# Kernel optimization log

Hardware: AMD Instinct MI355X
Metric: run time of the kernel (lower is better)

The kernel has to match this reference:

```python
import jax, jax.numpy as jnp
import numpy as np

N_NODES = 50000
NEG_SLOPE = 0.2
EPS = 1e-16


def _gat_layer(x, src, dst, W, a_src, a_dst, b, concat):
    """One PyG-style GATConv layer (eval mode, self-loops already in src/dst).
    x: [N, F_in], W: [F_in, H*C], a_src/a_dst: [H, C], b: [H*C] or [C].
    """
    H, C = a_src.shape
    N = x.shape[0]
    h = (x @ W).reshape(N, H, C)                      # [N, H, C]
    alpha_s = jnp.einsum('nhc,hc->nh', h, a_src)      # [N, H]
    alpha_d = jnp.einsum('nhc,hc->nh', h, a_dst)      # [N, H]
    e = alpha_s[src] + alpha_d[dst]                   # [E, H]
    e = jax.nn.leaky_relu(e, NEG_SLOPE)
    # segment softmax over edges grouped by destination node
    m = jax.ops.segment_max(e, dst, num_segments=N)   # [N, H]
    e = jnp.exp(e - m[dst])
    denom = jax.ops.segment_sum(e, dst, num_segments=N)
    alpha = e / (denom[dst] + EPS)                    # [E, H]
    msg = h[src] * alpha[:, :, None]                  # [E, H, C]
    out = jax.ops.segment_sum(msg, dst, num_segments=N)  # [N, H, C]
    if concat:
        out = out.reshape(N, H * C)
    else:
        out = out.mean(axis=1)
    return out + b


def setup_inputs() -> dict:
    key = jax.random.key(0)
    ks = jax.random.split(key, 16)
    N, E = N_NODES, 800000
    in_dim, hid, heads = 128, 64, 2
    x = jax.random.normal(ks[0], (N, in_dim), dtype=jnp.float32)
    edge_index = jax.random.randint(ks[1], (2, E), 0, N, dtype=jnp.int64)
    s = 0.1
    return {
        'x': x,
        'edge_index': edge_index,
        # layer 0: in_dim -> hid, heads
        'W0': s * jax.random.normal(ks[2], (in_dim, heads * hid), dtype=jnp.float32),
        'as0': s * jax.random.normal(ks[3], (heads, hid), dtype=jnp.float32),
        'ad0': s * jax.random.normal(ks[4], (heads, hid), dtype=jnp.float32),
        'b0': jnp.zeros((heads * hid,), dtype=jnp.float32),
        # layer 1: hid*heads -> hid, heads
        'W1': s * jax.random.normal(ks[5], (heads * hid, heads * hid), dtype=jnp.float32),
        'as1': s * jax.random.normal(ks[6], (heads, hid), dtype=jnp.float32),
        'ad1': s * jax.random.normal(ks[7], (heads, hid), dtype=jnp.float32),
        'b1': jnp.zeros((heads * hid,), dtype=jnp.float32),
        # layer 2: hid*heads -> hid, heads=1
        'W2': s * jax.random.normal(ks[8], (heads * hid, hid), dtype=jnp.float32),
        'as2': s * jax.random.normal(ks[9], (1, hid), dtype=jnp.float32),
        'ad2': s * jax.random.normal(ks[10], (1, hid), dtype=jnp.float32),
        'b2': jnp.zeros((hid,), dtype=jnp.float32),
    }


def reference(x, edge_index, W0, as0, ad0, b0, W1, as1, ad1, b1, W2, as2, ad2, b2):
    N = x.shape[0]
    # PyG GATConv default add_self_loops=True
    loop = jnp.arange(N, dtype=edge_index.dtype)
    src = jnp.concatenate([edge_index[0], loop])
    dst = jnp.concatenate([edge_index[1], loop])
    h = _gat_layer(x, src, dst, W0, as0, ad0, b0, concat=True)
    h = jax.nn.relu(h)
    h = _gat_layer(h, src, dst, W1, as1, ad1, b1, concat=True)
    h = jax.nn.relu(h)
    out = _gat_layer(h, src, dst, W2, as2, ad2, b2, concat=True)  # heads=1: concat == identity
    return out
```

## Files before the change

kernel.cpp:

```cpp
#include <hip/hip_runtime.h>
#include <hip/hip_fp16.h>

#define NEG_SLOPE 0.2f
#define EPSF 1e-16f

typedef _Float16 half8 __attribute__((ext_vector_type(8)));
typedef float floatx4 __attribute__((ext_vector_type(4)));

__global__ void to_half_kernel(const float* __restrict__ in, __half* __restrict__ out,
                               int n8) {
    int i = blockIdx.x * blockDim.x + threadIdx.x;
    if (i < n8) {
        float4 a = ((const float4*)in)[i * 2];
        float4 b = ((const float4*)in)[i * 2 + 1];
        __half2 hp[4];
        hp[0] = __floats2half2_rn(a.x, a.y);
        hp[1] = __floats2half2_rn(a.z, a.w);
        hp[2] = __floats2half2_rn(b.x, b.y);
        hp[3] = __floats2half2_rn(b.z, b.w);
        ((uint4*)out)[i] = *(uint4*)hp;
    }
}

template<int BN, int HEADS>
__global__ __launch_bounds__(256) void gemm_mfma(const __half* __restrict__ X,
                                                 const float* __restrict__ W,
                                                 const float* __restrict__ asrc,
                                                 const float* __restrict__ adst,
                                                 __half* __restrict__ OutH,
                                                 float* __restrict__ AS,
                                                 float* __restrict__ AD, int N) {
    constexpr int KP = 136;
    constexpr int NF = BN / 16;
    __shared__ _Float16 Wt[BN][KP];
    const int tid = threadIdx.x;
    const int wave = tid >> 6, lane = tid & 63;
    const int r = lane & 15;
    const int g = lane >> 4;
    const int row0 = blockIdx.x * 64 + wave * 16;

    for (int idx = tid; idx < 128 * (BN / 4); idx += 256) {
        int k = idx / (BN / 4), n4 = idx % (BN / 4);
        float4 w4 = *(const float4*)&W[(size_t)k * BN + n4 * 4];
        Wt[n4 * 4 + 0][k] = (_Float16)w4.x;
        Wt[n4 * 4 + 1][k] = (_Float16)w4.y;
        Wt[n4 * 4 + 2][k] = (_Float16)w4.z;
        Wt[n4 * 4 + 3][k] = (_Float16)w4.w;
    }
    __syncthreads();

    const int arow = row0 + r;
    const int arow_c = (arow < N) ? arow : (N - 1);

    floatx4 acc[NF];
#pragma unroll
    for (int n = 0; n < NF; ++n) acc[n] = (floatx4)(0.f);

#pragma unroll
    for (int ks = 0; ks < 4; ++ks) {
        half8 afrag = *(const half8*)&X[(size_t)arow_c * 128 + ks * 32 + g * 8];
#pragma unroll
        for (int n = 0; n < NF; ++n) {
            half8 bfrag = *(const half8*)&Wt[n * 16 + r][ks * 32 + g * 8];
            acc[n] = __builtin_amdgcn_mfma_f32_16x16x32_f16(afrag, bfrag, acc[n], 0, 0, 0);
        }
    }

    float av[NF], dv[NF];
#pragma unroll
    for (int n = 0; n < NF; ++n) { av[n] = asrc[n * 16 + r]; dv[n] = adst[n * 16 + r]; }

#pragma unroll
    for (int reg = 0; reg < 4; ++reg) {
        const int orow = row0 + g * 4 + reg;
        if (orow >= N) continue;
#pragma unroll
        for (int n = 0; n < NF; ++n)
            OutH[(size_t)orow * BN + n * 16 + r] = __float2half(acc[n][reg]);
        float ps0 = 0.f, pd0 = 0.f, ps1 = 0.f, pd1 = 0.f;
#pragma unroll
        for (int n = 0; n < NF; ++n) {
            float v = acc[n][reg];
            if (HEADS == 2 && n >= NF / 2) { ps1 = fmaf(v, av[n], ps1); pd1 = fmaf(v, dv[n], pd1); }
            else                           { ps0 = fmaf(v, av[n], ps0); pd0 = fmaf(v, dv[n], pd0); }
        }
#pragma unroll
        for (int o = 1; o < 16; o <<= 1) {
            ps0 += __shfl_xor(ps0, o, 64); pd0 += __shfl_xor(pd0, o, 64);
            if (HEADS == 2) { ps1 += __shfl_xor(ps1, o, 64); pd1 += __shfl_xor(pd1, o, 64); }
        }
        if (r == 0) {
            if (HEADS == 2) {
                AS[orow * 2] = ps0; AS[orow * 2 + 1] = ps1;
                AD[orow * 2] = pd0; AD[orow * 2 + 1] = pd1;
            } else {
                AS[orow] = ps0; AD[orow] = pd0;
            }
        }
    }
}

__global__ void zero_kernel(int* __restrict__ p, int n4) {
    int i = blockIdx.x * blockDim.x + threadIdx.x;
    if (i < n4) ((int4*)p)[i] = make_int4(0, 0, 0, 0);
}

__global__ void hist_part(const int* __restrict__ ei, int E_raw, int N,
                          int* __restrict__ cnt) {
    const int NPART = 8;
    const int part = blockIdx.x & (NPART - 1);
    const int gblocks = gridDim.x >> 3;
    const int grank = blockIdx.x >> 3;
    const int tid = grank * blockDim.x + threadIdx.x;
    const int nthr = gblocks * blockDim.x;
    const int E = E_raw + N;
    const int dlo = (int)(((long long)N * part) / NPART);
    const int dhi = (int)(((long long)N * (part + 1)) / NPART);
    for (int e = tid; e < E; e += nthr) {
        int d = (e < E_raw) ? ei[E_raw + e] : e - E_raw;
        if (d >= dlo && d < dhi) atomicAdd(&cnt[d], 1);
    }
}

__global__ __launch_bounds__(256) void scan_block(const int* __restrict__ cnt,
                                                  int* __restrict__ offs,
                                                  int* __restrict__ bsum, int N) {
    __shared__ int wsum[4];
    const int i = blockIdx.x * 256 + threadIdx.x;
    const int lane = threadIdx.x & 63, w = threadIdx.x >> 6;
    int v = (i < N) ? cnt[i] : 0;
    int incl = v;
    for (int o = 1; o < 64; o <<= 1) {
        int t = __shfl_up(incl, o, 64);
        if (lane >= o) incl += t;
    }
    if (lane == 63) wsum[w] = incl;
    __syncthreads();
    int prefix = 0;
    for (int k = 0; k < w; ++k) prefix += wsum[k];
    if (i < N) offs[i] = prefix + incl - v;
    if (threadIdx.x == 255) bsum[blockIdx.x] = prefix + incl;
}

__global__ __launch_bounds__(256) void scan_bsum(int* __restrict__ bsum, int nb) {
    __shared__ int wsum[4];
    const int lane = threadIdx.x & 63, w = threadIdx.x >> 6;
    int v = (threadIdx.x < nb) ? bsum[threadIdx.x] : 0;
    int incl = v;
    for (int o = 1; o < 64; o <<= 1) {
        int t = __shfl_up(incl, o, 64);
        if (lane >= o) incl += t;
    }
    if (lane == 63) wsum[w] = incl;
    __syncthreads();
    int prefix = 0;
    for (int k = 0; k < w; ++k) prefix += wsum[k];
    if (threadIdx.x < nb) bsum[threadIdx.x] = prefix + incl - v;
}

__global__ void scan_add(int* __restrict__ offs, const int* __restrict__ bsum,
                         int N, int E) {
    const int i = blockIdx.x * 256 + threadIdx.x;
    if (i < N) offs[i] += bsum[blockIdx.x];
    if (i == 0) offs[N] = E;
}

__global__ void scatter_edges_part(const int* __restrict__ ei, int E_raw, int N,
                                   int* __restrict__ cnt,
                                   const int* __restrict__ offs,
                                   int* __restrict__ csr_src) {
    const int NPART = 8;
    const int part = blockIdx.x & (NPART - 1);
    const int gblocks = gridDim.x >> 3;
    const int grank = blockIdx.x >> 3;
    const int tid = grank * blockDim.x + threadIdx.x;
    const int nthr = gblocks * blockDim.x;
    const int E = E_raw + N;
    const int dlo = (int)(((long long)N * part) / NPART);
    const int dhi = (int)(((long long)N * (part + 1)) / NPART);
    for (int e = tid; e < E; e += nthr) {
        int d = (e < E_raw) ? ei[E_raw + e] : e - E_raw;
        if (d >= dlo && d < dhi) {
            int s = (e < E_raw) ? ei[e] : d;
            int old = atomicSub(&cnt[d], 1);
            csr_src[offs[d] + old - 1] = s;
        }
    }
}

__global__ __launch_bounds__(256) void gat_csr2(const int* __restrict__ offs,
                                                const int* __restrict__ csr_src,
                                                const float* __restrict__ AS,
                                                const float* __restrict__ AD,
                                                const __half* __restrict__ H,
                                                const float* __restrict__ bias,
                                                __half* __restrict__ Out,
                                                int N, int do_relu) {
    __shared__ int   sS[4][64];
    __shared__ float sP0[4][64];
    __shared__ float sP1[4][64];
    const int lane = threadIdx.x & 63;
    const int w = threadIdx.x >> 6;
    const int wid = (int)((blockIdx.x * blockDim.x + threadIdx.x) >> 6);
    const int nw = (int)((gridDim.x * blockDim.x) >> 6);
    const int c = lane & 15;
    const int slot = lane >> 4;
    const int myh = c >> 3;
    int* const sSw = &sS[w][0];
    const float* const myp = myh ? &sP1[w][0] : &sP0[w][0];
    const float4 bA = *(const float4*)&bias[8 * c];
    const float4 bB = *(const float4*)&bias[8 * c + 4];

    for (int n = wid; n < N; n += nw) {
        const int s0 = offs[n], s1 = offs[n + 1];
        const int deg = s1 - s0;
        const float2 adv = *(const float2*)&AD[(size_t)n * 2];
        float dn0 = 0.f, dn1 = 0.f, p0 = 0.f, p1 = 0.f;
        int sreg = 0;
        for (int i = s0 + lane; i < s1; i += 64) {
            int s = csr_src[i];
            float2 a2 = *(const float2*)&AS[(size_t)s * 2];
            float e0 = a2.x + adv.x, e1 = a2.y + adv.y;
            e0 = e0 > 0.f ? e0 : NEG_SLOPE * e0;
            e1 = e1 > 0.f ? e1 : NEG_SLOPE * e1;
            float pe0 = __expf(e0), pe1 = __expf(e1);
            dn0 += pe0; dn1 += pe1;
            if (i == s0 + lane) { sreg = s; p0 = pe0; p1 = pe1; }
        }
        for (int o = 1; o < 64; o <<= 1) {
            dn0 += __shfl_xor(dn0, o, 64);
            dn1 += __shfl_xor(dn1, o, 64);
        }
        const float myinv = 1.f / ((myh ? dn1 : dn0) + EPSF);

        float a[8];
#pragma unroll
        for (int j = 0; j < 8; ++j) a[j] = 0.f;
        if (deg <= 64) {
            sSw[lane] = sreg;
            sP0[w][lane] = p0;
            sP1[w][lane] = p1;
            const int npc = (deg + 3) >> 2;
            int t = 0;
            for (; t + 4 <= npc; t += 4) {
                int ss[4]; float pw[4]; uint4 hv[4];
#pragma unroll
                for (int k = 0; k < 4; ++k) {
                    int idx = 4 * (t + k) + slot;
                    ss[k] = sSw[idx];
                    pw[k] = myp[idx];
                }
#pragma unroll
                for (int k = 0; k < 4; ++k)
                    hv[k] = *(const uint4*)&H[(size_t)ss[k] * 128 + 8 * c];
#pragma unroll
                for (int k = 0; k < 4; ++k) {
                    const __half2* h2 = (const __half2*)&hv[k];
#pragma unroll
                    for (int j = 0; j < 4; ++j) {
                        float2 f = __half22float2(h2[j]);
                        a[2 * j]     = fmaf(f.x, pw[k], a[2 * j]);
                        a[2 * j + 1] = fmaf(f.y, pw[k], a[2 * j + 1]);
                    }
                }
            }
            for (; t < npc; ++t) {
                int idx = 4 * t + slot;
                int s = sSw[idx];
                float pw = myp[idx];
                uint4 hv = *(const uint4*)&H[(size_t)s * 128 + 8 * c];
                const __half2* h2 = (const __half2*)&hv;
#pragma unroll
                for (int j = 0; j < 4; ++j) {
                    float2 f = __half22float2(h2[j]);
                    a[2 * j]     = fmaf(f.x, pw, a[2 * j]);
                    a[2 * j + 1] = fmaf(f.y, pw, a[2 * j + 1]);
                }
            }
        } else {
            const float advh = myh ? adv.y : adv.x;
            for (int i = s0 + slot; i < s1; i += 4) {
                int s = csr_src[i];
                float e = AS[(size_t)s * 2 + myh] + advh;
                e = e > 0.f ? e : NEG_SLOPE * e;
                float pw = __expf(e);
                uint4 hv = *(const uint4*)&H[(size_t)s * 128 + 8 * c];
                const __half2* h2 = (const __half2*)&hv;
#pragma unroll
                for (int j = 0; j < 4; ++j) {
                    float2 f = __half22float2(h2[j]);
                    a[2 * j]     = fmaf(f.x, pw, a[2 * j]);
                    a[2 * j + 1] = fmaf(f.y, pw, a[2 * j + 1]);
                }
            }
        }
#pragma unroll
        for (int j = 0; j < 8; ++j) {
            a[j] += __shfl_xor(a[j], 16, 64);
            a[j] += __shfl_xor(a[j], 32, 64);
        }
        if (lane < 16) {
            float o[8];
            o[0] = a[0] * myinv + bA.x; o[1] = a[1] * myinv + bA.y;
            o[2] = a[2] * myinv + bA.z; o[3] = a[3] * myinv + bA.w;
            o[4] = a[4] * myinv + bB.x; o[5] = a[5] * myinv + bB.y;
            o[6] = a[6] * myinv + bB.z; o[7] = a[7] * myinv + bB.w;
            if (do_relu) {
#pragma unroll
                for (int j = 0; j < 8; ++j) o[j] = fmaxf(o[j], 0.f);
            }
            __half2 hp[4];
#pragma unroll
            for (int j = 0; j < 4; ++j) hp[j] = __floats2half2_rn(o[2 * j], o[2 * j + 1]);
            *(uint4*)&Out[(size_t)n * 128 + 8 * c] = *(uint4*)hp;
        }
    }
}

__global__ __launch_bounds__(256) void gat_csr1(const int* __restrict__ offs,
                                                const int* __restrict__ csr_src,
                                                const float* __restrict__ AS,
                                                const float* __restrict__ AD,
                                                const __half* __restrict__ H,
                                                const float* __restrict__ bias,
                                                float* __restrict__ Out,
                                                int N, int do_relu) {
    __shared__ int   sS[4][64];
    __shared__ float sP[4][64];
    const int lane = threadIdx.x & 63;
    const int w = threadIdx.x >> 6;
    const int wid = (int)((blockIdx.x * blockDim.x + threadIdx.x) >> 6);
    const int nw = (int)((gridDim.x * blockDim.x) >> 6);
    const int c = lane & 15;
    const int slot = lane >> 4;
    int* const sSw = &sS[w][0];
    float* const sPw = &sP[w][0];
    const float4 b4 = *(const float4*)&bias[4 * c];

    for (int n = wid; n < N; n += nw) {
        const int s0 = offs[n], s1 = offs[n + 1];
        const int deg = s1 - s0;
        const float adv0 = AD[n];
        float dn0 = 0.f, p0 = 0.f;
        int sreg = 0;
        for (int i = s0 + lane; i < s1; i += 64) {
            int s = csr_src[i];
            float e0 = AS[s] + adv0;
            e0 = e0 > 0.f ? e0 : NEG_SLOPE * e0;
            float pe0 = __expf(e0);
            dn0 += pe0;
            if (i == s0 + lane) { sreg = s; p0 = pe0; }
        }
        for (int o = 1; o < 64; o <<= 1) dn0 += __shfl_xor(dn0, o, 64);
        const float inv0 = 1.f / (dn0 + EPSF);

        float a[4];
#pragma unroll
        for (int j = 0; j < 4; ++j) a[j] = 0.f;
        if (deg <= 64) {
            sSw[lane] = sreg;
            sPw[lane] = p0;
            const int npc = (deg + 3) >> 2;
            int t = 0;
            for (; t + 4 <= npc; t += 4) {
                int ss[4]; float pw[4]; uint2 hv[4];
#pragma unroll
                for (int k = 0; k < 4; ++k) {
                    int idx = 4 * (t + k) + slot;
                    ss[k] = sSw[idx];
                    pw[k] = sPw[idx];
                }
#pragma unroll
                for (int k = 0; k < 4; ++k)
                    hv[k] = *(const uint2*)&H[(size_t)ss[k] * 64 + 4 * c];
#pragma unroll
                for (int k = 0; k < 4; ++k) {
                    const __half2* h2 = (const __half2*)&hv[k];
                    float2 f01 = __half22float2(h2[0]);
                    float2 f23 = __half22float2(h2[1]);
                    a[0] = fmaf(f01.x, pw[k], a[0]);
                    a[1] = fmaf(f01.y, pw[k], a[1]);
                    a[2] = fmaf(f23.x, pw[k], a[2]);
                    a[3] = fmaf(f23.y, pw[k], a[3]);
                }
            }
            for (; t < npc; ++t) {
                int idx = 4 * t + slot;
                int s = sSw[idx];
                float pw = sPw[idx];
                uint2 hv = *(const uint2*)&H[(size_t)s * 64 + 4 * c];
                const __half2* h2 = (const __half2*)&hv;
                float2 f01 = __half22float2(h2[0]);
                float2 f23 = __half22float2(h2[1]);
                a[0] = fmaf(f01.x, pw, a[0]);
                a[1] = fmaf(f01.y, pw, a[1]);
                a[2] = fmaf(f23.x, pw, a[2]);
                a[3] = fmaf(f23.y, pw, a[3]);
            }
        } else {
            for (int i = s0 + slot; i < s1; i += 4) {
                int s = csr_src[i];
                float e = AS[s] + adv0;
                e = e > 0.f ? e : NEG_SLOPE * e;
                float pw = __expf(e);
                uint2 hv = *(const uint2*)&H[(size_t)s * 64 + 4 * c];
                const __half2* h2 = (const __half2*)&hv;
                float2 f01 = __half22float2(h2[0]);
                float2 f23 = __half22float2(h2[1]);
                a[0] = fmaf(f01.x, pw, a[0]);
                a[1] = fmaf(f01.y, pw, a[1]);
                a[2] = fmaf(f23.x, pw, a[2]);
                a[3] = fmaf(f23.y, pw, a[3]);
            }
        }
#pragma unroll
        for (int j = 0; j < 4; ++j) {
            a[j] += __shfl_xor(a[j], 16, 64);
            a[j] += __shfl_xor(a[j], 32, 64);
        }
        if (lane < 16) {
            float4 o;
            o.x = a[0] * inv0 + b4.x;
            o.y = a[1] * inv0 + b4.y;
            o.z = a[2] * inv0 + b4.z;
            o.w = a[3] * inv0 + b4.w;
            if (do_relu) {
                o.x = fmaxf(o.x, 0.f); o.y = fmaxf(o.y, 0.f);
                o.z = fmaxf(o.z, 0.f); o.w = fmaxf(o.w, 0.f);
            }
            *(float4*)&Out[(size_t)n * 64 + 4 * c] = o;
        }
    }
}

extern "C" void kernel_launch(void* const* d_in, const int* in_sizes, int n_in,
                              void* d_out, int out_size, void* d_ws, size_t ws_size,
                              hipStream_t stream) {
    const float* x   = (const float*)d_in[0];
    const int*   ei  = (const int*)d_in[1];
    const float* W0  = (const float*)d_in[2];
    const float* as0 = (const float*)d_in[3];
    const float* ad0 = (const float*)d_in[4];
    const float* b0  = (const float*)d_in[5];
    const float* W1  = (const float*)d_in[6];
    const float* as1 = (const float*)d_in[7];
    const float* ad1 = (const float*)d_in[8];
    const float* b1  = (const float*)d_in[9];
    const float* W2  = (const float*)d_in[10];
    const float* as2 = (const float*)d_in[11];
    const float* ad2 = (const float*)d_in[12];
    const float* b2  = (const float*)d_in[13];

    const int N = in_sizes[0] / 128;
    const int E_raw = in_sizes[1] / 2;
    const int E = E_raw + N;

    char* ws = (char*)d_ws;
    size_t off = 0;
    auto alloc = [&](size_t bytes) {
        void* p = ws + off;
        off = (off + bytes + 255) & ~(size_t)255;
        return p;
    };
    __half* xh    = (__half*)alloc((size_t)N * 128 * 2);
    __half* hh    = (__half*)alloc((size_t)N * 128 * 2);
    __half* obufh = (__half*)alloc((size_t)N * 128 * 2);
    float* asb  = (float*)alloc((size_t)N * 2 * 4);
    float* adb  = (float*)alloc((size_t)N * 2 * 4);
    int*   cnt  = (int*)alloc((size_t)(N + 4) * 4);
    int*   offs = (int*)alloc((size_t)(N + 1) * 4);
    int*   bsum = (int*)alloc(1024);
    int* csr_src = (int*)alloc((size_t)E * 4);
    (void)ws_size; (void)n_in; (void)out_size;

    const int nb = (N + 255) / 256;
    const int n4 = (N + 3) / 4;
    zero_kernel<<<(n4 + 255) / 256, 256, 0, stream>>>(cnt, n4);
    hist_part<<<2048, 256, 0, stream>>>(ei, E_raw, N, cnt);
    scan_block<<<nb, 256, 0, stream>>>(cnt, offs, bsum, N);
    scan_bsum<<<1, 256, 0, stream>>>(bsum, nb);
    scan_add<<<nb, 256, 0, stream>>>(offs, bsum, N, E);
    scatter_edges_part<<<2048, 256, 0, stream>>>(ei, E_raw, N, cnt, offs, csr_src);

    const int n8 = N * 128 / 8;
    to_half_kernel<<<(n8 + 255) / 256, 256, 0, stream>>>(x, xh, n8);

    const int gemm_blocks = (N + 63) / 64;
    const int gat_blocks = 2048;

    gemm_mfma<128, 2><<<gemm_blocks, 256, 0, stream>>>(xh, W0, as0, ad0, hh, asb, adb, N);
    gat_csr2<<<gat_blocks, 256, 0, stream>>>(offs, csr_src, asb, adb, hh, b0, obufh, N, 1);
    gemm_mfma<128, 2><<<gemm_blocks, 256, 0, stream>>>(obufh, W1, as1, ad1, hh, asb, adb, N);
    gat_csr2<<<gat_blocks, 256, 0, stream>>>(offs, csr_src, asb, adb, hh, b1, obufh, N, 1);
    gemm_mfma<64, 1><<<gemm_blocks, 256, 0, stream>>>(obufh, W2, as2, ad2, hh, asb, adb, N);
    gat_csr1<<<gat_blocks, 256, 0, stream>>>(offs, csr_src, asb, adb, hh, b2, (float*)d_out, N, 0);
}
```

Before: 257.2 us.

## Fuse CSR build into one cooperative kernel and fold fp16 conversion into GEMM

Replaces the six CSR-construction launches (zero, histogram, three scan stages, scatter) with a single cooperative kernel that separates the phases with grid-wide syncs. It also drops the separate float-to-half pass over x by converting fp32 rows to fp16 inside the first GEMM's A-fragment load. The aim is to cut launch overhead and one full read/write of the input matrix. In exchange, the grid is fixed at 1024 blocks, which must all be co-resident for the grid syncs, and the scan phase requires nb (196) to stay within the grid size.

```diff
diff --git a/kernel.cpp b/kernel.cpp
--- a/kernel.cpp
+++ b/kernel.cpp
@@ -1,5 +1,8 @@
 #include <hip/hip_runtime.h>
 #include <hip/hip_fp16.h>
+#include <hip/hip_cooperative_groups.h>
+
+namespace cg = cooperative_groups;
 
 #define NEG_SLOPE 0.2f
 #define EPSF 1e-16f
@@ -7,23 +10,8 @@
 typedef _Float16 half8 __attribute__((ext_vector_type(8)));
 typedef float floatx4 __attribute__((ext_vector_type(4)));
 
-__global__ void to_half_kernel(const float* __restrict__ in, __half* __restrict__ out,
-                               int n8) {
-    int i = blockIdx.x * blockDim.x + threadIdx.x;
-    if (i < n8) {
-        float4 a = ((const float4*)in)[i * 2];
-        float4 b = ((const float4*)in)[i * 2 + 1];
-        __half2 hp[4];
-        hp[0] = __floats2half2_rn(a.x, a.y);
-        hp[1] = __floats2half2_rn(a.z, a.w);
-        hp[2] = __floats2half2_rn(b.x, b.y);
-        hp[3] = __floats2half2_rn(b.z, b.w);
-        ((uint4*)out)[i] = *(uint4*)hp;
-    }
-}
-
-template<int BN, int HEADS>
-__global__ __launch_bounds__(256) void gemm_mfma(const __half* __restrict__ X,
+template<int BN, int HEADS, typename XT>
+__global__ __launch_bounds__(256) void gemm_mfma(const XT* __restrict__ X,
                                                  const float* __restrict__ W,
                                                  const float* __restrict__ asrc,
                                                  const float* __restrict__ adst,
@@ -58,7 +46,18 @@
 
 #pragma unroll
     for (int ks = 0; ks < 4; ++ks) {
-        half8 afrag = *(const half8*)&X[(size_t)arow_c * 128 + ks * 32 + g * 8];
+        half8 afrag;
+        if constexpr (sizeof(XT) == 2) {
+            afrag = *(const half8*)&X[(size_t)arow_c * 128 + ks * 32 + g * 8];
+        } else {
+            const float* xp = (const float*)&X[(size_t)arow_c * 128 + ks * 32 + g * 8];
+            float4 a = *(const float4*)xp;
+            float4 b = *(const float4*)(xp + 4);
+            afrag[0] = (_Float16)a.x; afrag[1] = (_Float16)a.y;
+            afrag[2] = (_Float16)a.z; afrag[3] = (_Float16)a.w;
+            afrag[4] = (_Float16)b.x; afrag[5] = (_Float16)b.y;
+            afrag[6] = (_Float16)b.z; afrag[7] = (_Float16)b.w;
+        }
 #pragma unroll
         for (int n = 0; n < NF; ++n) {
             half8 bfrag = *(const half8*)&Wt[n * 16 + r][ks * 32 + g * 8];
@@ -100,90 +99,91 @@
     }
 }
 
-__global__ void zero_kernel(int* __restrict__ p, int n4) {
-    int i = blockIdx.x * blockDim.x + threadIdx.x;
-    if (i < n4) ((int4*)p)[i] = make_int4(0, 0, 0, 0);
-}
-
-__global__ void hist_part(const int* __restrict__ ei, int E_raw, int N,
-                          int* __restrict__ cnt) {
-    const int NPART = 8;
-    const int part = blockIdx.x & (NPART - 1);
-    const int gblocks = gridDim.x >> 3;
-    const int grank = blockIdx.x >> 3;
-    const int tid = grank * blockDim.x + threadIdx.x;
-    const int nthr = gblocks * blockDim.x;
+__global__ void csr_build_coop(const int* __restrict__ ei, int E_raw, int N,
+                               int* __restrict__ cnt, int* __restrict__ offs,
+                               int* __restrict__ bsum, int* __restrict__ csr_src) {
+    cg::grid_group grid = cg::this_grid();
+    __shared__ int wsum[4];
+    const int tid = blockIdx.x * blockDim.x + threadIdx.x;
+    const int nthr = gridDim.x * blockDim.x;
     const int E = E_raw + N;
-    const int dlo = (int)(((long long)N * part) / NPART);
-    const int dhi = (int)(((long long)N * (part + 1)) / NPART);
-    for (int e = tid; e < E; e += nthr) {
-        int d = (e < E_raw) ? ei[E_raw + e] : e - E_raw;
-        if (d >= dlo && d < dhi) atomicAdd(&cnt[d], 1);
-    }
-}
-
-__global__ __launch_bounds__(256) void scan_block(const int* __restrict__ cnt,
-                                                  int* __restrict__ offs,
-                                                  int* __restrict__ bsum, int N) {
-    __shared__ int wsum[4];
-    const int i = blockIdx.x * 256 + threadIdx.x;
     const int lane = threadIdx.x & 63, w = threadIdx.x >> 6;
-    int v = (i < N) ? cnt[i] : 0;
-    int incl = v;
-    for (int o = 1; o < 64; o <<= 1) {
-        int t = __shfl_up(incl, o, 64);
-        if (lane >= o) incl += t;
-    }
-    if (lane == 63) wsum[w] = incl;
-    __syncthreads();
-    int prefix = 0;
-    for (int k = 0; k < w; ++k) prefix += wsum[k];
-    if (i < N) offs[i] = prefix + incl - v;
-    if (threadIdx.x == 255) bsum[blockIdx.x] = prefix + incl;
-}
-
-__global__ __launch_bounds__(256) void scan_bsum(int* __restrict__ bsum, int nb) {
-    __shared__ int wsum[4];
-    const int lane = threadIdx.x & 63, w = threadIdx.x >> 6;
-    int v = (threadIdx.x < nb) ? bsum[threadIdx.x] : 0;
-    int incl = v;
-    for (int o = 1; o < 64; o <<= 1) {
-        int t = __shfl_up(incl, o, 64);
-        if (lane >= o) incl += t;
-    }
-    if (lane == 63) wsum[w] = incl;
-    __syncthreads();
-    int prefix = 0;
-    for (int k = 0; k < w; ++k) prefix += wsum[k];
-    if (threadIdx.x < nb) bsum[threadIdx.x] = prefix + incl - v;
-}
-
-__global__ void scan_add(int* __restrict__ offs, const int* __restrict__ bsum,
-                         int N, int E) {
-    const int i = blockIdx.x * 256 + threadIdx.x;
-    if (i < N) offs[i] += bsum[blockIdx.x];
-    if (i == 0) offs[N] = E;
-}
-
-__global__ void scatter_edges_part(const int* __restrict__ ei, int E_raw, int N,
-                                   int* __restrict__ cnt,
-                                   const int* __restrict__ offs,
-                                   int* __restrict__ csr_src) {
-    const int NPART = 8;
-    const int part = blockIdx.x & (NPART - 1);
-    const int gblocks = gridDim.x >> 3;
-    const int grank = blockIdx.x >> 3;
-    const int tid = grank * blockDim.x + threadIdx.x;
-    const int nthr = gblocks * blockDim.x;
-    const int E = E_raw + N;
-    const int dlo = (int)(((long long)N * part) / NPART);
-    const int dhi = (int)(((long long)N * (part + 1)) / NPART);
-    for (int e = tid; e < E; e += nthr) {
-        int d = (e < E_raw) ? ei[E_raw + e] : e - E_raw;
-        if (d >= dlo && d < dhi) {
-            int s = (e < E_raw) ? ei[e] : d;
-            int old = atomicSub(&cnt[d], 1);
-            csr_src[offs[d] + old - 1] = s;
+    const int nb = (N + 255) / 256;
+
+    for (int i = tid; i < (N + 3) / 4; i += nthr)
+        ((int4*)cnt)[i] = make_int4(0, 0, 0, 0);
+    grid.sync();
+
+    {
+        const int part = blockIdx.x & 7;
+        const int grank = blockIdx.x >> 3;
+        const int gblocks = gridDim.x >> 3;
+        const int t2 = grank * blockDim.x + threadIdx.x;
+        const int n2 = gblocks * blockDim.x;
+        const int dlo = (int)(((long long)N * part) / 8);
+        const int dhi = (int)(((long long)N * (part + 1)) / 8);
+        for (int e = t2; e < E; e += n2) {
+            int d = (e < E_raw) ? ei[E_raw + e] : e - E_raw;
+            if (d >= dlo && d < dhi) atomicAdd(&cnt[d], 1);
+        }
+    }
+    grid.sync();
+
+    if (blockIdx.x < nb) {
+        const int i = blockIdx.x * 256 + threadIdx.x;
+        int v = (i < N) ? cnt[i] : 0;
+        int incl = v;
+        for (int o = 1; o < 64; o <<= 1) {
+            int t = __shfl_up(incl, o, 64);
+            if (lane >= o) incl += t;
+        }
+        if (lane == 63) wsum[w] = incl;
+        __syncthreads();
+        int prefix = 0;
+        for (int k = 0; k < w; ++k) prefix += wsum[k];
+        if (i < N) offs[i] = prefix + incl - v;
+        if (threadIdx.x == 255) bsum[blockIdx.x] = prefix + incl;
+        __syncthreads();
+    }
+    grid.sync();
+
+    if (blockIdx.x == 0) {
+        int v = (threadIdx.x < nb) ? bsum[threadIdx.x] : 0;
+        int incl = v;
+        for (int o = 1; o < 64; o <<= 1) {
+            int t = __shfl_up(incl, o, 64);
+            if (lane >= o) incl += t;
+        }
+        if (lane == 63) wsum[w] = incl;
+        __syncthreads();
+        int prefix = 0;
+        for (int k = 0; k < w; ++k) prefix += wsum[k];
+        if (threadIdx.x < nb) bsum[threadIdx.x] = prefix + incl - v;
+    }
+    grid.sync();
+
+    if (blockIdx.x < nb) {
+        const int i = blockIdx.x * 256 + threadIdx.x;
+        if (i < N) offs[i] += bsum[blockIdx.x];
+        if (i == 0) offs[N] = E;
+    }
+    grid.sync();
+
+    {
+        const int part = blockIdx.x & 7;
+        const int grank = blockIdx.x >> 3;
+        const int gblocks = gridDim.x >> 3;
+        const int t2 = grank * blockDim.x + threadIdx.x;
+        const int n2 = gblocks * blockDim.x;
+        const int dlo = (int)(((long long)N * part) / 8);
+        const int dhi = (int)(((long long)N * (part + 1)) / 8);
+        for (int e = t2; e < E; e += n2) {
+            int d = (e < E_raw) ? ei[E_raw + e] : e - E_raw;
+            if (d >= dlo && d < dhi) {
+                int s = (e < E_raw) ? ei[e] : d;
+                int old = atomicSub(&cnt[d], 1);
+                csr_src[offs[d] + old - 1] = s;
+            }
         }
     }
 }
@@ -462,7 +462,6 @@
         off = (off + bytes + 255) & ~(size_t)255;
         return p;
     };
-    __half* xh    = (__half*)alloc((size_t)N * 128 * 2);
     __half* hh    = (__half*)alloc((size_t)N * 128 * 2);
     __half* obufh = (__half*)alloc((size_t)N * 128 * 2);
     float* asb  = (float*)alloc((size_t)N * 2 * 4);
@@ -473,25 +472,21 @@
     int* csr_src = (int*)alloc((size_t)E * 4);
     (void)ws_size; (void)n_in; (void)out_size;
 
-    const int nb = (N + 255) / 256;
-    const int n4 = (N + 3) / 4;
-    zero_kernel<<<(n4 + 255) / 256, 256, 0, stream>>>(cnt, n4);
-    hist_part<<<2048, 256, 0, stream>>>(ei, E_raw, N, cnt);
-    scan_block<<<nb, 256, 0, stream>>>(cnt, offs, bsum, N);
-    scan_bsum<<<1, 256, 0, stream>>>(bsum, nb);
-    scan_add<<<nb, 256, 0, stream>>>(offs, bsum, N, E);
-    scatter_edges_part<<<2048, 256, 0, stream>>>(ei, E_raw, N, cnt, offs, csr_src);
-
-    const int n8 = N * 128 / 8;
-    to_half_kernel<<<(n8 + 255) / 256, 256, 0, stream>>>(x, xh, n8);
+    {
+        int* ei_p = (int*)ei;
+        void* args[] = { (void*)&ei_p, (void*)&E_raw, (void*)&N,
+                         (void*)&cnt, (void*)&offs, (void*)&bsum, (void*)&csr_src };
+        hipLaunchCooperativeKernel((void*)csr_build_coop, dim3(1024), dim3(256),
+                                   args, 0, stream);
+    }
 
     const int gemm_blocks = (N + 63) / 64;
     const int gat_blocks = 2048;
 
-    gemm_mfma<128, 2><<<gemm_blocks, 256, 0, stream>>>(xh, W0, as0, ad0, hh, asb, adb, N);
+    gemm_mfma<128, 2, float><<<gemm_blocks, 256, 0, stream>>>(x, W0, as0, ad0, hh, asb, adb, N);
     gat_csr2<<<gat_blocks, 256, 0, stream>>>(offs, csr_src, asb, adb, hh, b0, obufh, N, 1);
-    gemm_mfma<128, 2><<<gemm_blocks, 256, 0, stream>>>(obufh, W1, as1, ad1, hh, asb, adb, N);
+    gemm_mfma<128, 2, __half><<<gemm_blocks, 256, 0, stream>>>(obufh, W1, as1, ad1, hh, asb, adb, N);
     gat_csr2<<<gat_blocks, 256, 0, stream>>>(offs, csr_src, asb, adb, hh, b1, obufh, N, 1);
-    gemm_mfma<64, 1><<<gemm_blocks, 256, 0, stream>>>(obufh, W2, as2, ad2, hh, asb, adb, N);
+    gemm_mfma<64, 1, __half><<<gemm_blocks, 256, 0, stream>>>(obufh, W2, as2, ad2, hh, asb, adb, N);
     gat_csr1<<<gat_blocks, 256, 0, stream>>>(offs, csr_src, asb, adb, hh, b2, (float*)d_out, N, 0);
 }
```

Measured after the change: 711.9 us. 2.77x slower.
